# Kernel tuning notes

Hardware: AMD Instinct MI355X
Metric: run time of the kernel (lower is better)

Reference implementation:

```python
import jax, jax.numpy as jnp
import numpy as np

N_NODES, N_EDGES, HIDDEN, N_GRAPHS, TARGET, DEPTH, N_FOURIER = 20000, 320000, 128, 64, 32, 4, 4


def setup_inputs() -> dict:
    key = jax.random.key(0)
    ks = iter(jax.random.split(key, 48))
    H, L = HIDDEN, DEPTH

    def nrm(shape, fan):
        return jax.random.normal(next(ks), shape, jnp.float32) / np.sqrt(fan)

    inp = {}
    inp["x"] = jnp.zeros((N_NODES, 9), jnp.int32)  # only N is used (use_node_features=False)
    src = jax.random.randint(next(ks), (N_EDGES,), 0, N_NODES, dtype=jnp.int32)
    dst = jax.random.randint(next(ks), (N_EDGES,), 0, N_NODES, dtype=jnp.int32)
    inp["edge_index"] = jnp.stack([src, dst])  # row0 = x_j (source), row1 = x_i (target)
    inp["edge_attr"] = jax.random.uniform(next(ks), (N_EDGES,), jnp.float32) * 5.0  # distances
    inp["batch"] = ((jnp.arange(N_NODES) * N_GRAPHS) // N_NODES).astype(jnp.int32)  # sorted, all graphs non-empty

    ein = 2 * N_FOURIER + 1
    inp["node_embedding"] = jax.random.normal(next(ks), (H,), jnp.float32)
    inp["edge_W"] = nrm((ein, H), ein); inp["edge_b"] = jnp.zeros((H,), jnp.float32)
    # stacked per-mp-layer params (scanned over)
    inp["msg_W1"] = nrm((L, 3 * H, H), 3 * H); inp["msg_b1"] = jnp.zeros((L, H), jnp.float32)
    inp["msg_W2"] = nrm((L, H, H), H);        inp["msg_b2"] = jnp.zeros((L, H), jnp.float32)
    inp["soft_W"] = nrm((L, H, 1), H);        inp["soft_b"] = jnp.zeros((L, 1), jnp.float32)
    inp["upd_W1"] = nrm((L, H, H), H);        inp["upd_b1"] = jnp.zeros((L, H), jnp.float32)
    inp["upd_W2"] = nrm((L, H, H), H);        inp["upd_b2"] = jnp.zeros((L, H), jnp.float32)
    # node-wise output MLP (2 layers, last_activation=None)
    inp["no_W1"] = nrm((H, H), H); inp["no_b1"] = jnp.zeros((H,), jnp.float32)
    inp["no_W2"] = nrm((H, H), H); inp["no_b2"] = jnp.zeros((H,), jnp.float32)
    # readout MLP: in = 3*H (mean, sum, max), hidden = H, out = TARGET
    inp["out_W1"] = nrm((3 * H, H), 3 * H); inp["out_b1"] = jnp.zeros((H,), jnp.float32)
    inp["out_W2"] = nrm((H, TARGET), H);    inp["out_b2"] = jnp.zeros((TARGET,), jnp.float32)
    return inp


def _forward(x, edge_index, edge_attr, batch, node_embedding, edge_W, edge_b,
             msg_W1, msg_b1, msg_W2, msg_b2, soft_W, soft_b,
             upd_W1, upd_b1, upd_W2, upd_b2,
             no_W1, no_b1, no_W2, no_b2, out_W1, out_b1, out_W2, out_b2):
    N = x.shape[0]
    silu = jax.nn.silu
    h = jnp.broadcast_to(node_embedding, (N, node_embedding.shape[0]))

    # fourier_encode_dist: [E] -> [E, 2*F+1]
    scales = 2.0 ** jnp.arange(N_FOURIER, dtype=edge_attr.dtype)
    d = edge_attr[:, None] / scales
    e = jnp.concatenate([jnp.sin(d), jnp.cos(d), edge_attr[:, None]], axis=-1)
    # edge_input MLP (layers=1, last_activation=SiLU) followed by extra F.silu in forward
    e = silu(silu(e @ edge_W + edge_b))

    src, dst = edge_index[0], edge_index[1]  # x_j gathers src, x_i gathers dst

    def layer(carry, p):
        h, e = carry
        W1, b1, W2, b2, sW, sb, uW1, ub1, uW2, ub2 = p
        m_in = jnp.concatenate([h[src], h[dst], e], axis=-1)  # [x_j, x_i, edge_attr]
        m = silu(silu(m_in @ W1 + b1) @ W2 + b2)              # message MLP, last_activation=SiLU
        e = e + m                                             # in-place edge_attr += message
        w = jax.nn.sigmoid(m @ sW + sb)                       # soft edge gate
        agg = jax.ops.segment_sum(m * w, dst, num_segments=N) # aggr='sum' to targets
        hn = silu((agg + h) @ uW1 + ub1) @ uW2 + ub2          # update MLP, last_activation=None
        return (h + hn, e), None

    (h, e), _ = jax.lax.scan(layer, (h, e),
                             (msg_W1, msg_b1, msg_W2, msg_b2, soft_W, soft_b,
                              upd_W1, upd_b1, upd_W2, upd_b2))

    h = silu(h @ no_W1 + no_b1) @ no_W2 + no_b2  # node-wise output network

    G = N_GRAPHS
    s = jax.ops.segment_sum(h, batch, num_segments=G)
    cnt = jax.ops.segment_sum(jnp.ones((N, 1), h.dtype), batch, num_segments=G)
    mean = s / jnp.maximum(cnt, 1.0)
    mx = jax.ops.segment_max(h, batch, num_segments=G)
    readout = jnp.concatenate([mean, s, mx], axis=-1)  # aggregators = [mean, sum, max]
    return jax.nn.relu(readout @ out_W1 + out_b1) @ out_W2 + out_b2


def reference(x, edge_index, edge_attr, batch, node_embedding, edge_W, edge_b,
              msg_W1, msg_b1, msg_W2, msg_b2, soft_W, soft_b,
              upd_W1, upd_b1, upd_W2, upd_b2,
              no_W1, no_b1, no_W2, no_b2, out_W1, out_b1, out_W2, out_b2):
    return _forward(x, edge_index, edge_attr, batch, node_embedding, edge_W, edge_b,
                    msg_W1, msg_b1, msg_W2, msg_b2, soft_W, soft_b,
                    upd_W1, upd_b1, upd_W2, upd_b2,
                    no_W1, no_b1, no_W2, no_b2, out_W1, out_b1, out_W2, out_b2)
```

## Files before the change

### kernel.cpp

```cpp
#include <hip/hip_runtime.h>

#define N_NODES 20000
#define N_EDGES 320000
#define HID 128
#define NG 64
#define TGT 32
#define DEPTHL 4

typedef __attribute__((ext_vector_type(8))) short s16x8;
typedef __attribute__((ext_vector_type(4))) short s16x4;
typedef __attribute__((ext_vector_type(4))) float f32x4;

__device__ __forceinline__ unsigned short f2b(float f) {
  unsigned u = __builtin_bit_cast(unsigned, f);
  u = (u + 0x7FFFu + ((u >> 16) & 1u)) >> 16;
  return (unsigned short)u;
}
__device__ __forceinline__ float b2f(unsigned short s) {
  return __builtin_bit_cast(float, ((unsigned)s) << 16);
}
__device__ __forceinline__ float silu_f(float x) { return x / (1.f + __expf(-x)); }

__device__ __forceinline__ unsigned fkey(float f) {
  unsigned u = __builtin_bit_cast(unsigned, f);
  return (u & 0x80000000u) ? ~u : (u | 0x80000000u);
}
__device__ __forceinline__ float unkey(unsigned k) {
  unsigned u = (k & 0x80000000u) ? (k ^ 0x80000000u) : ~k;
  return __builtin_bit_cast(float, u);
}

__device__ __forceinline__ f32x4 mfma16(s16x8 a, s16x8 b, f32x4 c) {
  return __builtin_amdgcn_mfma_f32_16x16x32_bf16(a, b, c, 0, 0, 0);
}

__device__ __forceinline__ void lds_fence() {
  asm volatile("s_waitcnt lgkmcnt(0)" ::: "memory");
  __builtin_amdgcn_sched_barrier(0);
}

__device__ __forceinline__ s16x8 pack8(float4 a, float4 b) {
  s16x8 p;
  p[0]=(short)f2b(a.x); p[1]=(short)f2b(a.y); p[2]=(short)f2b(a.z); p[3]=(short)f2b(a.w);
  p[4]=(short)f2b(b.x); p[5]=(short)f2b(b.y); p[6]=(short)f2b(b.z); p[7]=(short)f2b(b.w);
  return p;
}

__global__ void pack_weights(const float* __restrict__ mW1, const float* __restrict__ mW2,
                             const float* __restrict__ uW1, const float* __restrict__ uW2,
                             const float* __restrict__ nW1, const float* __restrict__ nW2,
                             short* __restrict__ pW1, short* __restrict__ pW2,
                             short* __restrict__ puW1, short* __restrict__ puW2,
                             short* __restrict__ pnW1, short* __restrict__ pnW2) {
  int i = blockIdx.x * 256 + threadIdx.x;
  const float* src; short* dst; int K, r;
  if (i < 196608)      { src = mW1 + (i/49152)*49152; dst = pW1 + i;            r = i % 49152; K = 384; }
  else if (i < 262144) { int q = i - 196608; src = mW2 + (q/16384)*16384; dst = pW2  + q; r = q % 16384; K = 128; }
  else if (i < 327680) { int q = i - 262144; src = uW1 + (q/16384)*16384; dst = puW1 + q; r = q % 16384; K = 128; }
  else if (i < 393216) { int q = i - 327680; src = uW2 + (q/16384)*16384; dst = puW2 + q; r = q % 16384; K = 128; }
  else if (i < 409600) { int q = i - 393216; src = nW1; dst = pnW1 + q; r = q; K = 128; }
  else if (i < 425984) { int q = i - 409600; src = nW2; dst = pnW2 + q; r = q; K = 128; }
  else return;
  int j = r & 7, lane = (r >> 3) & 63, q2 = r >> 9;
  int KT = K >> 5;
  int kt = q2 % KT, ct = q2 / KT;
  int k = kt*32 + ((lane >> 4) << 3) + j;
  int col = ct*16 + (lane & 15);
  dst[0] = (short)f2b(src[k*HID + col]);
}

__global__ void sort_init(int* __restrict__ hist, int* __restrict__ cursor) {
  int i = blockIdx.x * 256 + threadIdx.x;
  if (i < N_NODES) { hist[i] = 0; cursor[i] = 0; }
}

__global__ void hist_kernel(const int* __restrict__ dst, int* __restrict__ hist) {
  int e = blockIdx.x * 256 + threadIdx.x;
  if (e < N_EDGES) atomicAdd(&hist[dst[e]], 1);
}

__global__ __launch_bounds__(1024) void scan_kernel(const int* __restrict__ hist,
                                                    int* __restrict__ offs) {
  __shared__ int part[1024];
  int t = threadIdx.x;
  int base = t * 20;
  int loc[20];
  int s = 0;
#pragma unroll
  for (int i = 0; i < 20; ++i) {
    loc[i] = s;
    int n = base + i;
    s += (n < N_NODES ? hist[n] : 0);
  }
  part[t] = s;
  __syncthreads();
  for (int st = 1; st < 1024; st <<= 1) {
    int v = (t >= st) ? part[t - st] : 0;
    __syncthreads();
    part[t] += v;
    __syncthreads();
  }
  int pre = (t > 0) ? part[t - 1] : 0;
#pragma unroll
  for (int i = 0; i < 20; ++i) {
    int n = base + i;
    if (n < N_NODES) offs[n] = pre + loc[i];
  }
}

__global__ void scatter_kernel(const int* __restrict__ src, const int* __restrict__ dst,
                               const float* __restrict__ ea, const int* __restrict__ offs,
                               int* __restrict__ cursor,
                               unsigned short* __restrict__ ssrc,
                               unsigned short* __restrict__ sdst,
                               float* __restrict__ sea) {
  int e = blockIdx.x * 256 + threadIdx.x;
  if (e >= N_EDGES) return;
  int d = dst[e];
  int pos = offs[d] + atomicAdd(&cursor[d], 1);
  ssrc[pos] = (unsigned short)src[e];
  sdst[pos] = (unsigned short)d;
  sea[pos] = ea[e];
}

__global__ void edge_init(const float* __restrict__ sea, const float* __restrict__ eW,
                          const float* __restrict__ eb, unsigned short* __restrict__ e) {
  __shared__ float feat[2][9];
  int t = threadIdx.x;
  int le = t >> 7, c = t & 127;
  int edge = blockIdx.x * 2 + le;
  if (c < 9) {
    float d = sea[edge];
    float sc = (float)(1 << (c & 3));
    float v;
    if (c < 4) v = sinf(d / sc);
    else if (c < 8) v = cosf(d / sc);
    else v = d;
    feat[le][c] = v;
  }
  __syncthreads();
  float acc = eb[c];
#pragma unroll
  for (int j = 0; j < 9; ++j) acc += feat[le][j] * eW[j*HID + c];
  acc = silu_f(silu_f(acc));
  e[edge*HID + c] = f2b(acc);
}

__global__ void init_h(float* __restrict__ h, const float* __restrict__ ne,
                       float* __restrict__ agg, unsigned short* __restrict__ hb) {
  int i = blockIdx.x * 256 + threadIdx.x;
  if (i < N_NODES * HID) {
    float v = ne[i & 127];
    h[i] = v; hb[i] = f2b(v); agg[i] = 0.f;
  }
}

__global__ void init_read(float* __restrict__ s, float* __restrict__ cnt, unsigned* __restrict__ mx) {
  int i = blockIdx.x * 256 + threadIdx.x;
  if (i < NG * HID) { s[i] = 0.f; mx[i] = 0x007FFFFFu; }
  if (i < NG) cnt[i] = 0.f;
}

__global__ __launch_bounds__(256) void msg_kernel(
    const unsigned short* __restrict__ hb, unsigned short* __restrict__ e,
    const unsigned short* __restrict__ ssrc, const unsigned short* __restrict__ sdst,
    const short* __restrict__ W1p, const float* __restrict__ b1,
    const short* __restrict__ W2p, const float* __restrict__ b2,
    const float* __restrict__ sW, const float* __restrict__ sbp,
    float* __restrict__ agg) {
  __shared__ __align__(16) short t1f[4][2048];
  int t = threadIdx.x;
  int wv = t >> 6, lane = t & 63;
  int l15 = lane & 15, hi = lane >> 4;
  int edge = blockIdx.x * 64 + wv * 16 + l15;
  int si = ssrc[edge];
  int d  = sdst[edge];

  s16x8 bfrag[12];
#pragma unroll
  for (int kt = 0; kt < 4; ++kt)
    bfrag[kt] = *(const s16x8*)(hb + si*HID + kt*32 + hi*8);
#pragma unroll
  for (int kt = 0; kt < 4; ++kt)
    bfrag[4+kt] = *(const s16x8*)(hb + d*HID + kt*32 + hi*8);
#pragma unroll
  for (int kt = 0; kt < 4; ++kt)
    bfrag[8+kt] = *(const s16x8*)(e + (size_t)edge*HID + kt*32 + hi*8);

  f32x4 acc1[8];
#pragma unroll
  for (int ct = 0; ct < 8; ++ct) acc1[ct] = f32x4{0.f, 0.f, 0.f, 0.f};
#pragma unroll
  for (int kt = 0; kt < 12; ++kt) {
#pragma unroll
    for (int ct = 0; ct < 8; ++ct) {
      s16x8 afr = *(const s16x8*)(W1p + ((ct*12 + kt)*64 + lane)*8);
      acc1[ct] = mfma16(afr, bfrag[kt], acc1[ct]);
    }
  }
  short* myt1 = &t1f[wv][0];
#pragma unroll
  for (int ct = 0; ct < 8; ++ct) {
    f32x4 bias = *(const f32x4*)(b1 + ct*16 + hi*4);
    s16x4 pk4;
#pragma unroll
    for (int r = 0; r < 4; ++r) pk4[r] = (short)f2b(silu_f(acc1[ct][r] + bias[r]));
    *(s16x4*)&myt1[((2*ct + (hi >> 1))*16 + l15)*8 + (hi & 1)*4] = pk4;
  }
  uint2 eold[8];
#pragma unroll
  for (int ct = 0; ct < 8; ++ct)
    eold[ct] = *(const uint2*)(e + (size_t)edge*HID + ct*16 + hi*4);
  lds_fence();

  f32x4 acc2[8];
#pragma unroll
  for (int ct = 0; ct < 8; ++ct) acc2[ct] = f32x4{0.f, 0.f, 0.f, 0.f};
#pragma unroll
  for (int kt = 0; kt < 4; ++kt) {
    s16x8 bfr = *(const s16x8*)&myt1[((kt*4 + hi)*16 + l15)*8];
#pragma unroll
    for (int ct = 0; ct < 8; ++ct) {
      s16x8 afr = *(const s16x8*)(W2p + ((ct*4 + kt)*64 + lane)*8);
      acc2[ct] = mfma16(afr, bfr, acc2[ct]);
    }
  }
  float m[8][4];
  float wpart = 0.f;
#pragma unroll
  for (int ct = 0; ct < 8; ++ct) {
    f32x4 bias = *(const f32x4*)(b2 + ct*16 + hi*4);
    f32x4 swv  = *(const f32x4*)(sW + ct*16 + hi*4);
#pragma unroll
    for (int r = 0; r < 4; ++r) {
      float mv = silu_f(acc2[ct][r] + bias[r]);
      m[ct][r] = mv;
      wpart += mv * swv[r];
    }
  }
  wpart += __shfl_xor(wpart, 16);
  wpart += __shfl_xor(wpart, 32);
  float wg = 1.f / (1.f + __expf(-(wpart + sbp[0])));

  int pd = __shfl_up(d, 1, 16);
  bool head = (l15 == 0) || (pd != d);
  int okbits = 0;
#pragma unroll
  for (int i = 0; i < 4; ++i) {
    int off = 1 << i;
    int nd = __shfl_down(d, off, 16);
    if ((l15 + off < 16) && (nd == d)) okbits |= (1 << i);
  }
  float* aggrow = agg + d*HID;

#pragma unroll
  for (int ct = 0; ct < 8; ++ct) {
    uint2 cur = eold[ct];
    float f0 = b2f((unsigned short)(cur.x & 0xFFFFu)) + m[ct][0];
    float f1 = b2f((unsigned short)(cur.x >> 16))     + m[ct][1];
    float f2v = b2f((unsigned short)(cur.y & 0xFFFFu)) + m[ct][2];
    float f3 = b2f((unsigned short)(cur.y >> 16))     + m[ct][3];
    uint2 nw;
    nw.x = (unsigned)f2b(f0)  | ((unsigned)f2b(f1) << 16);
    nw.y = (unsigned)f2b(f2v) | ((unsigned)f2b(f3) << 16);
    *(uint2*)(e + (size_t)edge*HID + ct*16 + hi*4) = nw;

    f32x4 v;
#pragma unroll
    for (int r = 0; r < 4; ++r) v[r] = m[ct][r] * wg;
#pragma unroll
    for (int i = 0; i < 4; ++i) {
      int off = 1 << i;
      bool ok = (okbits >> i) & 1;
#pragma unroll
      for (int r = 0; r < 4; ++r) {
        float nv = __shfl_down(v[r], off, 16);
        if (ok) v[r] += nv;
      }
    }
    if (head) {
      float* ap = aggrow + ct*16 + hi*4;
      atomicAdd(ap + 0, v[0]);
      atomicAdd(ap + 1, v[1]);
      atomicAdd(ap + 2, v[2]);
      atomicAdd(ap + 3, v[3]);
    }
  }
}

template<int MODE>
__global__ __launch_bounds__(256) void node_kernel(
    float* __restrict__ h, float* __restrict__ agg,
    const short* __restrict__ W1p, const float* __restrict__ b1,
    const short* __restrict__ W2p, const float* __restrict__ b2,
    float* __restrict__ out, unsigned short* __restrict__ hb) {
  __shared__ __align__(16) short t1f[4][2048];
  int t = threadIdx.x;
  int wv = t >> 6, lane = t & 63;
  int l15 = lane & 15, hi = lane >> 4;
  int node = blockIdx.x * 64 + wv * 16 + l15;
  bool valid = node < N_NODES;
  int nodec = valid ? node : (N_NODES - 1);

  s16x8 bfrag[4];
#pragma unroll
  for (int kt = 0; kt < 4; ++kt) {
    const float* hp = h + nodec*HID + kt*32 + hi*8;
    float4 v0 = *(const float4*)hp;
    float4 v1 = *(const float4*)(hp + 4);
    if (MODE == 0) {
      float* ap = agg + nodec*HID + kt*32 + hi*8;
      float4 a0 = *(const float4*)ap;
      float4 a1 = *(const float4*)(ap + 4);
      v0.x += a0.x; v0.y += a0.y; v0.z += a0.z; v0.w += a0.w;
      v1.x += a1.x; v1.y += a1.y; v1.z += a1.z; v1.w += a1.w;
      if (valid) {
        float4 z = {0.f, 0.f, 0.f, 0.f};
        *(float4*)ap = z;
        *(float4*)(ap + 4) = z;
      }
    }
    bfrag[kt] = pack8(v0, v1);
  }

  f32x4 acc1[8];
#pragma unroll
  for (int ct = 0; ct < 8; ++ct) acc1[ct] = f32x4{0.f, 0.f, 0.f, 0.f};
#pragma unroll
  for (int kt = 0; kt < 4; ++kt) {
#pragma unroll
    for (int ct = 0; ct < 8; ++ct) {
      s16x8 afr = *(const s16x8*)(W1p + ((ct*4 + kt)*64 + lane)*8);
      acc1[ct] = mfma16(afr, bfrag[kt], acc1[ct]);
    }
  }
  short* myt1 = &t1f[wv][0];
#pragma unroll
  for (int ct = 0; ct < 8; ++ct) {
    f32x4 bias = *(const f32x4*)(b1 + ct*16 + hi*4);
    s16x4 pk4;
#pragma unroll
    for (int r = 0; r < 4; ++r) pk4[r] = (short)f2b(silu_f(acc1[ct][r] + bias[r]));
    *(s16x4*)&myt1[((2*ct + (hi >> 1))*16 + l15)*8 + (hi & 1)*4] = pk4;
  }
  lds_fence();

  f32x4 acc2[8];
#pragma unroll
  for (int ct = 0; ct < 8; ++ct) acc2[ct] = f32x4{0.f, 0.f, 0.f, 0.f};
#pragma unroll
  for (int kt = 0; kt < 4; ++kt) {
    s16x8 bfr = *(const s16x8*)&myt1[((kt*4 + hi)*16 + l15)*8];
#pragma unroll
    for (int ct = 0; ct < 8; ++ct) {
      s16x8 afr = *(const s16x8*)(W2p + ((ct*4 + kt)*64 + lane)*8);
      acc2[ct] = mfma16(afr, bfr, acc2[ct]);
    }
  }
  if (valid) {
#pragma unroll
    for (int ct = 0; ct < 8; ++ct) {
      f32x4 bias = *(const f32x4*)(b2 + ct*16 + hi*4);
      float* op = (MODE == 0 ? h : out) + node*HID + ct*16 + hi*4;
      float4 res;
      if (MODE == 0) {
        float4 cur = *(const float4*)op;
        res.x = cur.x + acc2[ct][0] + bias[0];
        res.y = cur.y + acc2[ct][1] + bias[1];
        res.z = cur.z + acc2[ct][2] + bias[2];
        res.w = cur.w + acc2[ct][3] + bias[3];
      } else {
        res.x = acc2[ct][0] + bias[0];
        res.y = acc2[ct][1] + bias[1];
        res.z = acc2[ct][2] + bias[2];
        res.w = acc2[ct][3] + bias[3];
      }
      *(float4*)op = res;
      if (MODE == 0) {
        uint2 nb;
        nb.x = (unsigned)f2b(res.x) | ((unsigned)f2b(res.y) << 16);
        nb.y = (unsigned)f2b(res.z) | ((unsigned)f2b(res.w) << 16);
        *(uint2*)(hb + node*HID + ct*16 + hi*4) = nb;
      }
    }
  }
}

__global__ void accum_kernel(const float* __restrict__ h2, const int* __restrict__ batch,
                             float* __restrict__ s, float* __restrict__ cnt,
                             unsigned* __restrict__ mx) {
  int c = threadIdx.x & 127;
  int lr = threadIdx.x >> 7;
  int base = blockIdx.x * 64;
  int cur = -1; float sum = 0.f, mxv = -3.0e38f, count = 0.f;
  for (int i = 0; i < 32; ++i) {
    int node = base + lr + 2 * i;
    if (node >= N_NODES) break;
    int g = batch[node];
    if (g != cur) {
      if (cur >= 0) {
        atomicAdd(&s[cur*HID + c], sum);
        atomicMax(&mx[cur*HID + c], fkey(mxv));
        if (c == 0) atomicAdd(&cnt[cur], count);
      }
      cur = g; sum = 0.f; mxv = -3.0e38f; count = 0.f;
    }
    float v = h2[node*HID + c];
    sum += v; mxv = fmaxf(mxv, v); count += 1.f;
  }
  if (cur >= 0) {
    atomicAdd(&s[cur*HID + c], sum);
    atomicMax(&mx[cur*HID + c], fkey(mxv));
    if (c == 0) atomicAdd(&cnt[cur], count);
  }
}

__global__ void final_kernel(const float* __restrict__ s, const float* __restrict__ cnt,
                             const unsigned* __restrict__ mx,
                             const float* __restrict__ W1, const float* __restrict__ b1,
                             const float* __restrict__ W2, const float* __restrict__ b2,
                             float* __restrict__ out) {
  __shared__ float ro[3 * HID];
  __shared__ float r1[HID];
  int g = blockIdx.x, c = threadIdx.x;
  float sv = s[g*HID + c];
  float cn = cnt[g];
  ro[c] = sv / fmaxf(cn, 1.f);
  ro[HID + c] = sv;
  ro[2*HID + c] = unkey(mx[g*HID + c]);
  __syncthreads();
  float acc = b1[c];
  for (int k = 0; k < 3*HID; ++k) acc += ro[k] * W1[k*HID + c];
  r1[c] = fmaxf(acc, 0.f);
  __syncthreads();
  if (c < TGT) {
    float o = b2[c];
    for (int k = 0; k < HID; ++k) o += r1[k] * W2[k*TGT + c];
    out[g*TGT + c] = o;
  }
}

extern "C" void kernel_launch(void* const* d_in, const int* in_sizes, int n_in,
                              void* d_out, int out_size, void* d_ws, size_t ws_size,
                              hipStream_t stream) {
  const int*   eidx = (const int*)d_in[1];
  const int*   srci = eidx;
  const int*   dsti = eidx + N_EDGES;
  const float* ea   = (const float*)d_in[2];
  const int*   batch= (const int*)d_in[3];
  const float* nemb = (const float*)d_in[4];
  const float* eW   = (const float*)d_in[5];
  const float* eb   = (const float*)d_in[6];
  const float* mW1  = (const float*)d_in[7];
  const float* mb1  = (const float*)d_in[8];
  const float* mW2  = (const float*)d_in[9];
  const float* mb2  = (const float*)d_in[10];
  const float* sW   = (const float*)d_in[11];
  const float* sb   = (const float*)d_in[12];
  const float* uW1  = (const float*)d_in[13];
  const float* ub1  = (const float*)d_in[14];
  const float* uW2  = (const float*)d_in[15];
  const float* ub2  = (const float*)d_in[16];
  const float* nW1  = (const float*)d_in[17];
  const float* nb1  = (const float*)d_in[18];
  const float* nW2  = (const float*)d_in[19];
  const float* nb2  = (const float*)d_in[20];
  const float* oW1  = (const float*)d_in[21];
  const float* ob1  = (const float*)d_in[22];
  const float* oW2  = (const float*)d_in[23];
  const float* ob2  = (const float*)d_in[24];

  char* ws = (char*)d_ws;
  float* sbuf = (float*)(ws + 0);
  float* cnt  = (float*)(ws + 32768);
  unsigned* mx= (unsigned*)(ws + 33024);
  short* pW1  = (short*)(ws + 65792);
  short* pW2  = (short*)(ws + 459008);
  short* puW1 = (short*)(ws + 590080);
  short* puW2 = (short*)(ws + 721152);
  short* pnW1 = (short*)(ws + 852224);
  short* pnW2 = (short*)(ws + 884992);
  int* hist   = (int*)(ws + 917760);
  int* cursor = (int*)(ws + 997760);
  int* offs   = (int*)(ws + 1077760);
  unsigned short* ssrc = (unsigned short*)(ws + 1157760);
  unsigned short* sdst = (unsigned short*)(ws + 1797760);
  float* sea  = (float*)(ws + 2437760);
  unsigned short* e = (unsigned short*)(ws + 3717760);
  float* h    = (float*)(ws + 85637760);
  float* agg  = (float*)(ws + 95877760);
  unsigned short* hb = (unsigned short*)(ws + 106117760);
  float* h2   = agg;

  sort_init<<<(N_NODES + 255) / 256, 256, 0, stream>>>(hist, cursor);
  hist_kernel<<<N_EDGES / 256, 256, 0, stream>>>(dsti, hist);
  scan_kernel<<<1, 1024, 0, stream>>>(hist, offs);
  scatter_kernel<<<N_EDGES / 256, 256, 0, stream>>>(srci, dsti, ea, offs, cursor,
                                                    ssrc, sdst, sea);

  pack_weights<<<1664, 256, 0, stream>>>(mW1, mW2, uW1, uW2, nW1, nW2,
                                         pW1, pW2, puW1, puW2, pnW1, pnW2);
  edge_init<<<N_EDGES / 2, 256, 0, stream>>>(sea, eW, eb, e);
  init_h<<<(N_NODES * HID) / 256, 256, 0, stream>>>(h, nemb, agg, hb);
  init_read<<<33, 256, 0, stream>>>(sbuf, cnt, mx);

  for (int l = 0; l < DEPTHL; ++l) {
    msg_kernel<<<N_EDGES / 64, 256, 0, stream>>>(hb, e, ssrc, sdst,
        pW1 + l*49152, mb1 + l*HID, pW2 + l*16384, mb2 + l*HID,
        sW + l*HID, sb + l, agg);
    node_kernel<0><<<(N_NODES + 63) / 64, 256, 0, stream>>>(h, agg,
        puW1 + l*16384, ub1 + l*HID, puW2 + l*16384, ub2 + l*HID, nullptr, hb);
  }
  node_kernel<1><<<(N_NODES + 63) / 64, 256, 0, stream>>>(h, nullptr,
      pnW1, nb1, pnW2, nb2, h2, nullptr);
  accum_kernel<<<(N_NODES + 63) / 64, 256, 0, stream>>>(h2, batch, sbuf, cnt, mx);
  final_kernel<<<NG, 128, 0, stream>>>(sbuf, cnt, mx, oW1, ob1, oW2, ob2, (float*)d_out);
}
```

Measured before the change: 979.4 us.

## Make message kernel persistent with LDS-resident weights and double-buffered edge loads

The message kernel now launches 256 blocks of 512 threads. Each block first copies the packed bf16 W1/W2 of the layer (144 KB, now stored contiguously per layer) into shared memory. Each wave then processes 10 consecutive 16-edge tiles, prefetching the gathered node and edge fragments of the next tile while the current one computes. This replaces the per-MFMA global/L2 weight fragment reads and spreads the weight load over many tiles. The cost is a large LDS footprint that allows only one block per CU, very low wave occupancy, high register pressure from the two fragment buffers, and a second-layer MFMA split into halves to fit a smaller per-wave staging buffer.

```diff
diff --git a/kernel.cpp b/kernel.cpp
--- a/kernel.cpp
+++ b/kernel.cpp
@@ -6,6 +6,7 @@
 #define NG 64
 #define TGT 32
 #define DEPTHL 4
+#define NTILES 20000
 
 typedef __attribute__((ext_vector_type(8))) short s16x8;
 typedef __attribute__((ext_vector_type(4))) short s16x4;
@@ -49,13 +50,13 @@
 __global__ void pack_weights(const float* __restrict__ mW1, const float* __restrict__ mW2,
                              const float* __restrict__ uW1, const float* __restrict__ uW2,
                              const float* __restrict__ nW1, const float* __restrict__ nW2,
-                             short* __restrict__ pW1, short* __restrict__ pW2,
+                             short* __restrict__ pMsg,
                              short* __restrict__ puW1, short* __restrict__ puW2,
                              short* __restrict__ pnW1, short* __restrict__ pnW2) {
   int i = blockIdx.x * 256 + threadIdx.x;
   const float* src; short* dst; int K, r;
-  if (i < 196608)      { src = mW1 + (i/49152)*49152; dst = pW1 + i;            r = i % 49152; K = 384; }
-  else if (i < 262144) { int q = i - 196608; src = mW2 + (q/16384)*16384; dst = pW2  + q; r = q % 16384; K = 128; }
+  if (i < 196608)      { int l = i/49152; r = i % 49152; src = mW1 + l*49152; dst = pMsg + l*65536 + r;        K = 384; }
+  else if (i < 262144) { int q = i - 196608; int l = q/16384; r = q % 16384; src = mW2 + l*16384; dst = pMsg + l*65536 + 49152 + r; K = 128; }
   else if (i < 327680) { int q = i - 262144; src = uW1 + (q/16384)*16384; dst = puW1 + q; r = q % 16384; K = 128; }
   else if (i < 393216) { int q = i - 327680; src = uW2 + (q/16384)*16384; dst = puW2 + q; r = q % 16384; K = 128; }
   else if (i < 409600) { int q = i - 393216; src = nW1; dst = pnW1 + q; r = q; K = 128; }
@@ -161,130 +162,172 @@
   if (i < NG) cnt[i] = 0.f;
 }
 
-__global__ __launch_bounds__(256) void msg_kernel(
+__global__ __launch_bounds__(512, 2) void msg_kernel(
     const unsigned short* __restrict__ hb, unsigned short* __restrict__ e,
     const unsigned short* __restrict__ ssrc, const unsigned short* __restrict__ sdst,
-    const short* __restrict__ W1p, const float* __restrict__ b1,
-    const short* __restrict__ W2p, const float* __restrict__ b2,
+    const short* __restrict__ Wp, const float* __restrict__ b1,
+    const float* __restrict__ b2,
     const float* __restrict__ sW, const float* __restrict__ sbp,
     float* __restrict__ agg) {
-  __shared__ __align__(16) short t1f[4][2048];
+  __shared__ __align__(16) short smem[73728];
+  short* sW1 = smem;
+  short* sW2 = smem + 49152;
   int t = threadIdx.x;
   int wv = t >> 6, lane = t & 63;
   int l15 = lane & 15, hi = lane >> 4;
-  int edge = blockIdx.x * 64 + wv * 16 + l15;
-  int si = ssrc[edge];
-  int d  = sdst[edge];
-
-  s16x8 bfrag[12];
-#pragma unroll
-  for (int kt = 0; kt < 4; ++kt)
-    bfrag[kt] = *(const s16x8*)(hb + si*HID + kt*32 + hi*8);
-#pragma unroll
-  for (int kt = 0; kt < 4; ++kt)
-    bfrag[4+kt] = *(const s16x8*)(hb + d*HID + kt*32 + hi*8);
-#pragma unroll
-  for (int kt = 0; kt < 4; ++kt)
-    bfrag[8+kt] = *(const s16x8*)(e + (size_t)edge*HID + kt*32 + hi*8);
-
-  f32x4 acc1[8];
-#pragma unroll
-  for (int ct = 0; ct < 8; ++ct) acc1[ct] = f32x4{0.f, 0.f, 0.f, 0.f};
-#pragma unroll
-  for (int kt = 0; kt < 12; ++kt) {
+  short* myt1 = smem + 65536 + wv * 1024;
+
+  {
+    const s16x8* Wg = (const s16x8*)Wp;
+    s16x8* Wl = (s16x8*)smem;
+    for (int i = t; i < 8192; i += 512) Wl[i] = Wg[i];
+  }
+  __syncthreads();
+
+  float sb_v = sbp[0];
+  int wgid = blockIdx.x * 8 + wv;
+  int tile0 = wgid * 10;
+
+  s16x8 bfA[12], bfB[12];
+  int dA = 0, dB = 0;
+
+  auto loadb = [&](s16x8* B, int& D, int tile) {
+    int edge = tile * 16 + l15;
+    int si = ssrc[edge]; D = sdst[edge];
+#pragma unroll
+    for (int kt = 0; kt < 4; ++kt)
+      B[kt] = *(const s16x8*)(hb + si*HID + kt*32 + hi*8);
+#pragma unroll
+    for (int kt = 0; kt < 4; ++kt)
+      B[4+kt] = *(const s16x8*)(hb + D*HID + kt*32 + hi*8);
+#pragma unroll
+    for (int kt = 0; kt < 4; ++kt)
+      B[8+kt] = *(const s16x8*)(e + (size_t)edge*HID + kt*32 + hi*8);
+  };
+
+  auto body = [&](int tile, const s16x8* bfrag, int d) {
+    int edge = tile * 16 + l15;
+    uint2 eold[8];
+#pragma unroll
+    for (int ct = 0; ct < 8; ++ct)
+      eold[ct] = *(const uint2*)(e + (size_t)edge*HID + ct*16 + hi*4);
+
+    f32x4 acc1[8];
+#pragma unroll
+    for (int ct = 0; ct < 8; ++ct) acc1[ct] = f32x4{0.f, 0.f, 0.f, 0.f};
+#pragma unroll
+    for (int kt = 0; kt < 12; ++kt) {
+#pragma unroll
+      for (int ct = 0; ct < 8; ++ct) {
+        s16x8 afr = *(const s16x8*)&sW1[((ct*12 + kt)*64 + lane)*8];
+        acc1[ct] = mfma16(afr, bfrag[kt], acc1[ct]);
+      }
+    }
+
+    f32x4 acc2[8];
+#pragma unroll
+    for (int ct = 0; ct < 8; ++ct) acc2[ct] = f32x4{0.f, 0.f, 0.f, 0.f};
+#pragma unroll
+    for (int p = 0; p < 2; ++p) {
+#pragma unroll
+      for (int c4 = 0; c4 < 4; ++c4) {
+        int ct = 4*p + c4;
+        f32x4 bias = *(const f32x4*)(b1 + ct*16 + hi*4);
+        s16x4 pk4;
+#pragma unroll
+        for (int r = 0; r < 4; ++r) pk4[r] = (short)f2b(silu_f(acc1[ct][r] + bias[r]));
+        *(s16x4*)&myt1[((2*c4 + (hi >> 1))*16 + l15)*8 + (hi & 1)*4] = pk4;
+      }
+      lds_fence();
+#pragma unroll
+      for (int k2 = 0; k2 < 2; ++k2) {
+        int kt = 2*p + k2;
+        s16x8 bfr = *(const s16x8*)&myt1[((k2*4 + hi)*16 + l15)*8];
+#pragma unroll
+        for (int ct = 0; ct < 8; ++ct) {
+          s16x8 afr = *(const s16x8*)&sW2[((ct*4 + kt)*64 + lane)*8];
+          acc2[ct] = mfma16(afr, bfr, acc2[ct]);
+        }
+      }
+      lds_fence();
+    }
+
+    float m[8][4];
+    float wpart = 0.f;
 #pragma unroll
     for (int ct = 0; ct < 8; ++ct) {
-      s16x8 afr = *(const s16x8*)(W1p + ((ct*12 + kt)*64 + lane)*8);
-      acc1[ct] = mfma16(afr, bfrag[kt], acc1[ct]);
-    }
-  }
-  short* myt1 = &t1f[wv][0];
-#pragma unroll
-  for (int ct = 0; ct < 8; ++ct) {
-    f32x4 bias = *(const f32x4*)(b1 + ct*16 + hi*4);
-    s16x4 pk4;
-#pragma unroll
-    for (int r = 0; r < 4; ++r) pk4[r] = (short)f2b(silu_f(acc1[ct][r] + bias[r]));
-    *(s16x4*)&myt1[((2*ct + (hi >> 1))*16 + l15)*8 + (hi & 1)*4] = pk4;
-  }
-  uint2 eold[8];
-#pragma unroll
-  for (int ct = 0; ct < 8; ++ct)
-    eold[ct] = *(const uint2*)(e + (size_t)edge*HID + ct*16 + hi*4);
-  lds_fence();
-
-  f32x4 acc2[8];
-#pragma unroll
-  for (int ct = 0; ct < 8; ++ct) acc2[ct] = f32x4{0.f, 0.f, 0.f, 0.f};
-#pragma unroll
-  for (int kt = 0; kt < 4; ++kt) {
-    s16x8 bfr = *(const s16x8*)&myt1[((kt*4 + hi)*16 + l15)*8];
-#pragma unroll
-    for (int ct = 0; ct < 8; ++ct) {
-      s16x8 afr = *(const s16x8*)(W2p + ((ct*4 + kt)*64 + lane)*8);
-      acc2[ct] = mfma16(afr, bfr, acc2[ct]);
-    }
-  }
-  float m[8][4];
-  float wpart = 0.f;
-#pragma unroll
-  for (int ct = 0; ct < 8; ++ct) {
-    f32x4 bias = *(const f32x4*)(b2 + ct*16 + hi*4);
-    f32x4 swv  = *(const f32x4*)(sW + ct*16 + hi*4);
-#pragma unroll
-    for (int r = 0; r < 4; ++r) {
-      float mv = silu_f(acc2[ct][r] + bias[r]);
-      m[ct][r] = mv;
-      wpart += mv * swv[r];
-    }
-  }
-  wpart += __shfl_xor(wpart, 16);
-  wpart += __shfl_xor(wpart, 32);
-  float wg = 1.f / (1.f + __expf(-(wpart + sbp[0])));
-
-  int pd = __shfl_up(d, 1, 16);
-  bool head = (l15 == 0) || (pd != d);
-  int okbits = 0;
-#pragma unroll
-  for (int i = 0; i < 4; ++i) {
-    int off = 1 << i;
-    int nd = __shfl_down(d, off, 16);
-    if ((l15 + off < 16) && (nd == d)) okbits |= (1 << i);
-  }
-  float* aggrow = agg + d*HID;
-
-#pragma unroll
-  for (int ct = 0; ct < 8; ++ct) {
-    uint2 cur = eold[ct];
-    float f0 = b2f((unsigned short)(cur.x & 0xFFFFu)) + m[ct][0];
-    float f1 = b2f((unsigned short)(cur.x >> 16))     + m[ct][1];
-    float f2v = b2f((unsigned short)(cur.y & 0xFFFFu)) + m[ct][2];
-    float f3 = b2f((unsigned short)(cur.y >> 16))     + m[ct][3];
-    uint2 nw;
-    nw.x = (unsigned)f2b(f0)  | ((unsigned)f2b(f1) << 16);
-    nw.y = (unsigned)f2b(f2v) | ((unsigned)f2b(f3) << 16);
-    *(uint2*)(e + (size_t)edge*HID + ct*16 + hi*4) = nw;
-
-    f32x4 v;
-#pragma unroll
-    for (int r = 0; r < 4; ++r) v[r] = m[ct][r] * wg;
+      f32x4 bias = *(const f32x4*)(b2 + ct*16 + hi*4);
+      f32x4 swv  = *(const f32x4*)(sW + ct*16 + hi*4);
+#pragma unroll
+      for (int r = 0; r < 4; ++r) {
+        float mv = silu_f(acc2[ct][r] + bias[r]);
+        m[ct][r] = mv;
+        wpart += mv * swv[r];
+      }
+    }
+    wpart += __shfl_xor(wpart, 16);
+    wpart += __shfl_xor(wpart, 32);
+    float wg = 1.f / (1.f + __expf(-(wpart + sb_v)));
+
+    int pd = __shfl_up(d, 1, 16);
+    bool head = (l15 == 0) || (pd != d);
+    int okbits = 0;
 #pragma unroll
     for (int i = 0; i < 4; ++i) {
       int off = 1 << i;
-      bool ok = (okbits >> i) & 1;
-#pragma unroll
-      for (int r = 0; r < 4; ++r) {
-        float nv = __shfl_down(v[r], off, 16);
-        if (ok) v[r] += nv;
-      }
-    }
-    if (head) {
-      float* ap = aggrow + ct*16 + hi*4;
-      atomicAdd(ap + 0, v[0]);
-      atomicAdd(ap + 1, v[1]);
-      atomicAdd(ap + 2, v[2]);
-      atomicAdd(ap + 3, v[3]);
-    }
+      int nd = __shfl_down(d, off, 16);
+      if ((l15 + off < 16) && (nd == d)) okbits |= (1 << i);
+    }
+    float* aggrow = agg + d*HID;
+
+#pragma unroll
+    for (int ct = 0; ct < 8; ++ct) {
+      uint2 cur = eold[ct];
+      float f0 = b2f((unsigned short)(cur.x & 0xFFFFu)) + m[ct][0];
+      float f1 = b2f((unsigned short)(cur.x >> 16))     + m[ct][1];
+      float f2v = b2f((unsigned short)(cur.y & 0xFFFFu)) + m[ct][2];
+      float f3 = b2f((unsigned short)(cur.y >> 16))     + m[ct][3];
+      uint2 nw;
+      nw.x = (unsigned)f2b(f0)  | ((unsigned)f2b(f1) << 16);
+      nw.y = (unsigned)f2b(f2v) | ((unsigned)f2b(f3) << 16);
+      *(uint2*)(e + (size_t)edge*HID + ct*16 + hi*4) = nw;
+
+      f32x4 v;
+#pragma unroll
+      for (int r = 0; r < 4; ++r) v[r] = m[ct][r] * wg;
+#pragma unroll
+      for (int i = 0; i < 4; ++i) {
+        int off = 1 << i;
+        bool ok = (okbits >> i) & 1;
+#pragma unroll
+        for (int r = 0; r < 4; ++r) {
+          float nv = __shfl_down(v[r], off, 16);
+          if (ok) v[r] += nv;
+        }
+      }
+      if (head) {
+        float* ap = aggrow + ct*16 + hi*4;
+        atomicAdd(ap + 0, v[0]);
+        atomicAdd(ap + 1, v[1]);
+        atomicAdd(ap + 2, v[2]);
+        atomicAdd(ap + 3, v[3]);
+      }
+    }
+  };
+
+  if (tile0 >= NTILES) return;
+  loadb(bfA, dA, tile0);
+#pragma unroll 1
+  for (int i = 0; i < 10; i += 2) {
+    int ta = tile0 + i;
+    if (ta >= NTILES) break;
+    int tb = ta + 1;
+    if (tb < NTILES && tb < tile0 + 10) loadb(bfB, dB, tb);
+    body(ta, bfA, dA);
+    if (tb >= NTILES || tb >= tile0 + 10) break;
+    int tc = tb + 1;
+    if (tc < NTILES && tc < tile0 + 10) loadb(bfA, dA, tc);
+    body(tb, bfB, dB);
   }
 }
 
@@ -474,8 +517,7 @@
   float* sbuf = (float*)(ws + 0);
   float* cnt  = (float*)(ws + 32768);
   unsigned* mx= (unsigned*)(ws + 33024);
-  short* pW1  = (short*)(ws + 65792);
-  short* pW2  = (short*)(ws + 459008);
+  short* pMsg = (short*)(ws + 65792);
   short* puW1 = (short*)(ws + 590080);
   short* puW2 = (short*)(ws + 721152);
   short* pnW1 = (short*)(ws + 852224);
@@ -499,14 +541,14 @@
                                                     ssrc, sdst, sea);
 
   pack_weights<<<1664, 256, 0, stream>>>(mW1, mW2, uW1, uW2, nW1, nW2,
-                                         pW1, pW2, puW1, puW2, pnW1, pnW2);
+                                         pMsg, puW1, puW2, pnW1, pnW2);
   edge_init<<<N_EDGES / 2, 256, 0, stream>>>(sea, eW, eb, e);
   init_h<<<(N_NODES * HID) / 256, 256, 0, stream>>>(h, nemb, agg, hb);
   init_read<<<33, 256, 0, stream>>>(sbuf, cnt, mx);
 
   for (int l = 0; l < DEPTHL; ++l) {
-    msg_kernel<<<N_EDGES / 64, 256, 0, stream>>>(hb, e, ssrc, sdst,
-        pW1 + l*49152, mb1 + l*HID, pW2 + l*16384, mb2 + l*HID,
+    msg_kernel<<<256, 512, 0, stream>>>(hb, e, ssrc, sdst,
+        pMsg + l*65536, mb1 + l*HID, mb2 + l*HID,
         sW + l*HID, sb + l, agg);
     node_kernel<0><<<(N_NODES + 63) / 64, 256, 0, stream>>>(h, agg,
         puW1 + l*16384, ub1 + l*HID, puW2 + l*16384, ub2 + l*HID, nullptr, hb);
```

Measured after the change: 930.4 us. -5.0%, faster.

## Replace atomic scatter aggregation with per-edge message buffer and CSR gather

Applied to the files above, without the earlier changes.

The message kernel no longer reduces within a segment and issues float atomics into a node aggregate buffer. It instead writes each gated message as bf16 to a per-edge buffer in destination-sorted order. The node kernel then gathers each node's incoming messages using the CSR offsets and degrees. This removes the atomics and the zeroing of the aggregate buffer, at the cost of an extra 80MB bf16 write and read per layer, bf16 rounding of messages before summation, and divergent per-node degree loops. The msg W1 and W2 packed weights are also merged into one contiguous per-layer block.

```diff
diff --git a/kernel.cpp b/kernel.cpp
--- a/kernel.cpp
+++ b/kernel.cpp
@@ -49,13 +49,13 @@
 __global__ void pack_weights(const float* __restrict__ mW1, const float* __restrict__ mW2,
                              const float* __restrict__ uW1, const float* __restrict__ uW2,
                              const float* __restrict__ nW1, const float* __restrict__ nW2,
-                             short* __restrict__ pW1, short* __restrict__ pW2,
+                             short* __restrict__ pMsg,
                              short* __restrict__ puW1, short* __restrict__ puW2,
                              short* __restrict__ pnW1, short* __restrict__ pnW2) {
   int i = blockIdx.x * 256 + threadIdx.x;
   const float* src; short* dst; int K, r;
-  if (i < 196608)      { src = mW1 + (i/49152)*49152; dst = pW1 + i;            r = i % 49152; K = 384; }
-  else if (i < 262144) { int q = i - 196608; src = mW2 + (q/16384)*16384; dst = pW2  + q; r = q % 16384; K = 128; }
+  if (i < 196608)      { int l = i/49152; r = i % 49152; src = mW1 + l*49152; dst = pMsg + l*65536 + r;        K = 384; }
+  else if (i < 262144) { int q = i - 196608; int l = q/16384; r = q % 16384; src = mW2 + l*16384; dst = pMsg + l*65536 + 49152 + r; K = 128; }
   else if (i < 327680) { int q = i - 262144; src = uW1 + (q/16384)*16384; dst = puW1 + q; r = q % 16384; K = 128; }
   else if (i < 393216) { int q = i - 327680; src = uW2 + (q/16384)*16384; dst = puW2 + q; r = q % 16384; K = 128; }
   else if (i < 409600) { int q = i - 393216; src = nW1; dst = pnW1 + q; r = q; K = 128; }
@@ -147,11 +147,11 @@
 }
 
 __global__ void init_h(float* __restrict__ h, const float* __restrict__ ne,
-                       float* __restrict__ agg, unsigned short* __restrict__ hb) {
+                       unsigned short* __restrict__ hb) {
   int i = blockIdx.x * 256 + threadIdx.x;
   if (i < N_NODES * HID) {
     float v = ne[i & 127];
-    h[i] = v; hb[i] = f2b(v); agg[i] = 0.f;
+    h[i] = v; hb[i] = f2b(v);
   }
 }
 
@@ -164,11 +164,13 @@
 __global__ __launch_bounds__(256) void msg_kernel(
     const unsigned short* __restrict__ hb, unsigned short* __restrict__ e,
     const unsigned short* __restrict__ ssrc, const unsigned short* __restrict__ sdst,
-    const short* __restrict__ W1p, const float* __restrict__ b1,
-    const short* __restrict__ W2p, const float* __restrict__ b2,
+    const short* __restrict__ Wp, const float* __restrict__ b1,
+    const float* __restrict__ b2,
     const float* __restrict__ sW, const float* __restrict__ sbp,
-    float* __restrict__ agg) {
+    unsigned short* __restrict__ mw) {
   __shared__ __align__(16) short t1f[4][2048];
+  const short* W1p = Wp;
+  const short* W2p = Wp + 49152;
   int t = threadIdx.x;
   int wv = t >> 6, lane = t & 63;
   int l15 = lane & 15, hi = lane >> 4;
@@ -241,17 +243,6 @@
   wpart += __shfl_xor(wpart, 16);
   wpart += __shfl_xor(wpart, 32);
   float wg = 1.f / (1.f + __expf(-(wpart + sbp[0])));
-
-  int pd = __shfl_up(d, 1, 16);
-  bool head = (l15 == 0) || (pd != d);
-  int okbits = 0;
-#pragma unroll
-  for (int i = 0; i < 4; ++i) {
-    int off = 1 << i;
-    int nd = __shfl_down(d, off, 16);
-    if ((l15 + off < 16) && (nd == d)) okbits |= (1 << i);
-  }
-  float* aggrow = agg + d*HID;
 
 #pragma unroll
   for (int ct = 0; ct < 8; ++ct) {
@@ -265,32 +256,17 @@
     nw.y = (unsigned)f2b(f2v) | ((unsigned)f2b(f3) << 16);
     *(uint2*)(e + (size_t)edge*HID + ct*16 + hi*4) = nw;
 
-    f32x4 v;
-#pragma unroll
-    for (int r = 0; r < 4; ++r) v[r] = m[ct][r] * wg;
-#pragma unroll
-    for (int i = 0; i < 4; ++i) {
-      int off = 1 << i;
-      bool ok = (okbits >> i) & 1;
-#pragma unroll
-      for (int r = 0; r < 4; ++r) {
-        float nv = __shfl_down(v[r], off, 16);
-        if (ok) v[r] += nv;
-      }
-    }
-    if (head) {
-      float* ap = aggrow + ct*16 + hi*4;
-      atomicAdd(ap + 0, v[0]);
-      atomicAdd(ap + 1, v[1]);
-      atomicAdd(ap + 2, v[2]);
-      atomicAdd(ap + 3, v[3]);
-    }
+    uint2 wout;
+    wout.x = (unsigned)f2b(m[ct][0]*wg) | ((unsigned)f2b(m[ct][1]*wg) << 16);
+    wout.y = (unsigned)f2b(m[ct][2]*wg) | ((unsigned)f2b(m[ct][3]*wg) << 16);
+    *(uint2*)(mw + (size_t)edge*HID + ct*16 + hi*4) = wout;
   }
 }
 
 template<int MODE>
 __global__ __launch_bounds__(256) void node_kernel(
-    float* __restrict__ h, float* __restrict__ agg,
+    float* __restrict__ h, const unsigned short* __restrict__ mw,
+    const int* __restrict__ offs, const int* __restrict__ hist,
     const short* __restrict__ W1p, const float* __restrict__ b1,
     const short* __restrict__ W2p, const float* __restrict__ b2,
     float* __restrict__ out, unsigned short* __restrict__ hb) {
@@ -303,24 +279,45 @@
   int nodec = valid ? node : (N_NODES - 1);
 
   s16x8 bfrag[4];
-#pragma unroll
-  for (int kt = 0; kt < 4; ++kt) {
-    const float* hp = h + nodec*HID + kt*32 + hi*8;
-    float4 v0 = *(const float4*)hp;
-    float4 v1 = *(const float4*)(hp + 4);
-    if (MODE == 0) {
-      float* ap = agg + nodec*HID + kt*32 + hi*8;
-      float4 a0 = *(const float4*)ap;
-      float4 a1 = *(const float4*)(ap + 4);
-      v0.x += a0.x; v0.y += a0.y; v0.z += a0.z; v0.w += a0.w;
-      v1.x += a1.x; v1.y += a1.y; v1.z += a1.z; v1.w += a1.w;
-      if (valid) {
-        float4 z = {0.f, 0.f, 0.f, 0.f};
-        *(float4*)ap = z;
-        *(float4*)(ap + 4) = z;
+  if (MODE == 0) {
+    int beg = offs[nodec];
+    int deg = valid ? hist[nodec] : 0;
+    int dmax = deg;
+#pragma unroll
+    for (int o = 32; o; o >>= 1) dmax = max(dmax, __shfl_xor(dmax, o));
+    float sum[4][8];
+#pragma unroll
+    for (int kt = 0; kt < 4; ++kt)
+#pragma unroll
+      for (int j = 0; j < 8; ++j) sum[kt][j] = 0.f;
+    for (int j = 0; j < dmax; ++j) {
+      if (j < deg) {
+        size_t row = (size_t)(beg + j) * HID;
+#pragma unroll
+        for (int kt = 0; kt < 4; ++kt) {
+          s16x8 v = *(const s16x8*)(mw + row + kt*32 + hi*8);
+#pragma unroll
+          for (int q = 0; q < 8; ++q) sum[kt][q] += b2f((unsigned short)v[q]);
+        }
       }
     }
-    bfrag[kt] = pack8(v0, v1);
+#pragma unroll
+    for (int kt = 0; kt < 4; ++kt) {
+      const float* hp = h + nodec*HID + kt*32 + hi*8;
+      float4 v0 = *(const float4*)hp;
+      float4 v1 = *(const float4*)(hp + 4);
+      v0.x += sum[kt][0]; v0.y += sum[kt][1]; v0.z += sum[kt][2]; v0.w += sum[kt][3];
+      v1.x += sum[kt][4]; v1.y += sum[kt][5]; v1.z += sum[kt][6]; v1.w += sum[kt][7];
+      bfrag[kt] = pack8(v0, v1);
+    }
+  } else {
+#pragma unroll
+    for (int kt = 0; kt < 4; ++kt) {
+      const float* hp = h + nodec*HID + kt*32 + hi*8;
+      float4 v0 = *(const float4*)hp;
+      float4 v1 = *(const float4*)(hp + 4);
+      bfrag[kt] = pack8(v0, v1);
+    }
   }
 
   f32x4 acc1[8];
@@ -474,8 +471,7 @@
   float* sbuf = (float*)(ws + 0);
   float* cnt  = (float*)(ws + 32768);
   unsigned* mx= (unsigned*)(ws + 33024);
-  short* pW1  = (short*)(ws + 65792);
-  short* pW2  = (short*)(ws + 459008);
+  short* pMsg = (short*)(ws + 65792);
   short* puW1 = (short*)(ws + 590080);
   short* puW2 = (short*)(ws + 721152);
   short* pnW1 = (short*)(ws + 852224);
@@ -488,9 +484,9 @@
   float* sea  = (float*)(ws + 2437760);
   unsigned short* e = (unsigned short*)(ws + 3717760);
   float* h    = (float*)(ws + 85637760);
-  float* agg  = (float*)(ws + 95877760);
-  unsigned short* hb = (unsigned short*)(ws + 106117760);
-  float* h2   = agg;
+  unsigned short* hb = (unsigned short*)(ws + 95877760);
+  unsigned short* mw = (unsigned short*)(ws + 100997760);
+  float* h2   = (float*)mw;
 
   sort_init<<<(N_NODES + 255) / 256, 256, 0, stream>>>(hist, cursor);
   hist_kernel<<<N_EDGES / 256, 256, 0, stream>>>(dsti, hist);
@@ -499,19 +495,19 @@
                                                     ssrc, sdst, sea);
 
   pack_weights<<<1664, 256, 0, stream>>>(mW1, mW2, uW1, uW2, nW1, nW2,
-                                         pW1, pW2, puW1, puW2, pnW1, pnW2);
+                                         pMsg, puW1, puW2, pnW1, pnW2);
   edge_init<<<N_EDGES / 2, 256, 0, stream>>>(sea, eW, eb, e);
-  init_h<<<(N_NODES * HID) / 256, 256, 0, stream>>>(h, nemb, agg, hb);
+  init_h<<<(N_NODES * HID) / 256, 256, 0, stream>>>(h, nemb, hb);
   init_read<<<33, 256, 0, stream>>>(sbuf, cnt, mx);
 
   for (int l = 0; l < DEPTHL; ++l) {
     msg_kernel<<<N_EDGES / 64, 256, 0, stream>>>(hb, e, ssrc, sdst,
-        pW1 + l*49152, mb1 + l*HID, pW2 + l*16384, mb2 + l*HID,
-        sW + l*HID, sb + l, agg);
-    node_kernel<0><<<(N_NODES + 63) / 64, 256, 0, stream>>>(h, agg,
+        pMsg + l*65536, mb1 + l*HID, mb2 + l*HID,
+        sW + l*HID, sb + l, mw);
+    node_kernel<0><<<(N_NODES + 63) / 64, 256, 0, stream>>>(h, mw, offs, hist,
         puW1 + l*16384, ub1 + l*HID, puW2 + l*16384, ub2 + l*HID, nullptr, hb);
   }
-  node_kernel<1><<<(N_NODES + 63) / 64, 256, 0, stream>>>(h, nullptr,
+  node_kernel<1><<<(N_NODES + 63) / 64, 256, 0, stream>>>(h, nullptr, nullptr, nullptr,
       pnW1, nb1, pnW2, nb2, h2, nullptr);
   accum_kernel<<<(N_NODES + 63) / 64, 256, 0, stream>>>(h2, batch, sbuf, cnt, mx);
   final_kernel<<<NG, 128, 0, stream>>>(sbuf, cnt, mx, oW1, ob1, oW2, ob2, (float*)d_out);
```

Measured after the change: 1.009 ms. 3.0% more time.

## Cut msg_kernel register pressure to raise occupancy and merge per-layer message weights

Applied to the files above, without the earlier changes.

The message kernel now loads the three 128-wide input chunks (source, destination, edge) in turn instead of holding all twelve fragments at once. It also defers the old-edge reload until after the second GEMM and recomputes the silu messages rather than keeping a 32-float array, and asks for 8 waves per EU via launch bounds. The per-layer W1 and W2 packed weights are placed in one contiguous buffer. This aims to raise occupancy and hide gather latency, at the cost of recomputed silu, less load-level parallelism per wave, and possible spills under the tighter register cap.

```diff
diff --git a/kernel.cpp b/kernel.cpp
--- a/kernel.cpp
+++ b/kernel.cpp
@@ -49,13 +49,13 @@
 __global__ void pack_weights(const float* __restrict__ mW1, const float* __restrict__ mW2,
                              const float* __restrict__ uW1, const float* __restrict__ uW2,
                              const float* __restrict__ nW1, const float* __restrict__ nW2,
-                             short* __restrict__ pW1, short* __restrict__ pW2,
+                             short* __restrict__ pMsg,
                              short* __restrict__ puW1, short* __restrict__ puW2,
                              short* __restrict__ pnW1, short* __restrict__ pnW2) {
   int i = blockIdx.x * 256 + threadIdx.x;
   const float* src; short* dst; int K, r;
-  if (i < 196608)      { src = mW1 + (i/49152)*49152; dst = pW1 + i;            r = i % 49152; K = 384; }
-  else if (i < 262144) { int q = i - 196608; src = mW2 + (q/16384)*16384; dst = pW2  + q; r = q % 16384; K = 128; }
+  if (i < 196608)      { int l = i/49152; r = i % 49152; src = mW1 + l*49152; dst = pMsg + l*65536 + r;        K = 384; }
+  else if (i < 262144) { int q = i - 196608; int l = q/16384; r = q % 16384; src = mW2 + l*16384; dst = pMsg + l*65536 + 49152 + r; K = 128; }
   else if (i < 327680) { int q = i - 262144; src = uW1 + (q/16384)*16384; dst = puW1 + q; r = q % 16384; K = 128; }
   else if (i < 393216) { int q = i - 327680; src = uW2 + (q/16384)*16384; dst = puW2 + q; r = q % 16384; K = 128; }
   else if (i < 409600) { int q = i - 393216; src = nW1; dst = pnW1 + q; r = q; K = 128; }
@@ -161,14 +161,16 @@
   if (i < NG) cnt[i] = 0.f;
 }
 
-__global__ __launch_bounds__(256) void msg_kernel(
+__global__ __launch_bounds__(256, 8) void msg_kernel(
     const unsigned short* __restrict__ hb, unsigned short* __restrict__ e,
     const unsigned short* __restrict__ ssrc, const unsigned short* __restrict__ sdst,
-    const short* __restrict__ W1p, const float* __restrict__ b1,
-    const short* __restrict__ W2p, const float* __restrict__ b2,
+    const short* __restrict__ Wp, const float* __restrict__ b1,
+    const float* __restrict__ b2,
     const float* __restrict__ sW, const float* __restrict__ sbp,
     float* __restrict__ agg) {
   __shared__ __align__(16) short t1f[4][2048];
+  const short* W1p = Wp;
+  const short* W2p = Wp + 49152;
   int t = threadIdx.x;
   int wv = t >> 6, lane = t & 63;
   int l15 = lane & 15, hi = lane >> 4;
@@ -176,28 +178,44 @@
   int si = ssrc[edge];
   int d  = sdst[edge];
 
-  s16x8 bfrag[12];
-#pragma unroll
-  for (int kt = 0; kt < 4; ++kt)
-    bfrag[kt] = *(const s16x8*)(hb + si*HID + kt*32 + hi*8);
-#pragma unroll
-  for (int kt = 0; kt < 4; ++kt)
-    bfrag[4+kt] = *(const s16x8*)(hb + d*HID + kt*32 + hi*8);
-#pragma unroll
-  for (int kt = 0; kt < 4; ++kt)
-    bfrag[8+kt] = *(const s16x8*)(e + (size_t)edge*HID + kt*32 + hi*8);
-
   f32x4 acc1[8];
 #pragma unroll
   for (int ct = 0; ct < 8; ++ct) acc1[ct] = f32x4{0.f, 0.f, 0.f, 0.f};
-#pragma unroll
-  for (int kt = 0; kt < 12; ++kt) {
-#pragma unroll
-    for (int ct = 0; ct < 8; ++ct) {
-      s16x8 afr = *(const s16x8*)(W1p + ((ct*12 + kt)*64 + lane)*8);
-      acc1[ct] = mfma16(afr, bfrag[kt], acc1[ct]);
-    }
-  }
+
+  {
+    s16x8 bf[4];
+#pragma unroll
+    for (int kt = 0; kt < 4; ++kt)
+      bf[kt] = *(const s16x8*)(hb + si*HID + kt*32 + hi*8);
+#pragma unroll
+    for (int kt = 0; kt < 4; ++kt)
+#pragma unroll
+      for (int ct = 0; ct < 8; ++ct)
+        acc1[ct] = mfma16(*(const s16x8*)(W1p + ((ct*12 + kt)*64 + lane)*8), bf[kt], acc1[ct]);
+  }
+  {
+    s16x8 bf[4];
+#pragma unroll
+    for (int kt = 0; kt < 4; ++kt)
+      bf[kt] = *(const s16x8*)(hb + d*HID + kt*32 + hi*8);
+#pragma unroll
+    for (int kt = 0; kt < 4; ++kt)
+#pragma unroll
+      for (int ct = 0; ct < 8; ++ct)
+        acc1[ct] = mfma16(*(const s16x8*)(W1p + ((ct*12 + kt + 4)*64 + lane)*8), bf[kt], acc1[ct]);
+  }
+  {
+    s16x8 bf[4];
+#pragma unroll
+    for (int kt = 0; kt < 4; ++kt)
+      bf[kt] = *(const s16x8*)(e + (size_t)edge*HID + kt*32 + hi*8);
+#pragma unroll
+    for (int kt = 0; kt < 4; ++kt)
+#pragma unroll
+      for (int ct = 0; ct < 8; ++ct)
+        acc1[ct] = mfma16(*(const s16x8*)(W1p + ((ct*12 + kt + 8)*64 + lane)*8), bf[kt], acc1[ct]);
+  }
+
   short* myt1 = &t1f[wv][0];
 #pragma unroll
   for (int ct = 0; ct < 8; ++ct) {
@@ -207,10 +225,6 @@
     for (int r = 0; r < 4; ++r) pk4[r] = (short)f2b(silu_f(acc1[ct][r] + bias[r]));
     *(s16x4*)&myt1[((2*ct + (hi >> 1))*16 + l15)*8 + (hi & 1)*4] = pk4;
   }
-  uint2 eold[8];
-#pragma unroll
-  for (int ct = 0; ct < 8; ++ct)
-    eold[ct] = *(const uint2*)(e + (size_t)edge*HID + ct*16 + hi*4);
   lds_fence();
 
   f32x4 acc2[8];
@@ -225,18 +239,20 @@
       acc2[ct] = mfma16(afr, bfr, acc2[ct]);
     }
   }
-  float m[8][4];
+
+  uint2 eold[8];
+#pragma unroll
+  for (int ct = 0; ct < 8; ++ct)
+    eold[ct] = *(const uint2*)(e + (size_t)edge*HID + ct*16 + hi*4);
+
   float wpart = 0.f;
 #pragma unroll
   for (int ct = 0; ct < 8; ++ct) {
     f32x4 bias = *(const f32x4*)(b2 + ct*16 + hi*4);
     f32x4 swv  = *(const f32x4*)(sW + ct*16 + hi*4);
 #pragma unroll
-    for (int r = 0; r < 4; ++r) {
-      float mv = silu_f(acc2[ct][r] + bias[r]);
-      m[ct][r] = mv;
-      wpart += mv * swv[r];
-    }
+    for (int r = 0; r < 4; ++r)
+      wpart += silu_f(acc2[ct][r] + bias[r]) * swv[r];
   }
   wpart += __shfl_xor(wpart, 16);
   wpart += __shfl_xor(wpart, 32);
@@ -255,11 +271,16 @@
 
 #pragma unroll
   for (int ct = 0; ct < 8; ++ct) {
+    f32x4 bias = *(const f32x4*)(b2 + ct*16 + hi*4);
+    f32x4 mv;
+#pragma unroll
+    for (int r = 0; r < 4; ++r) mv[r] = silu_f(acc2[ct][r] + bias[r]);
+
     uint2 cur = eold[ct];
-    float f0 = b2f((unsigned short)(cur.x & 0xFFFFu)) + m[ct][0];
-    float f1 = b2f((unsigned short)(cur.x >> 16))     + m[ct][1];
-    float f2v = b2f((unsigned short)(cur.y & 0xFFFFu)) + m[ct][2];
-    float f3 = b2f((unsigned short)(cur.y >> 16))     + m[ct][3];
+    float f0 = b2f((unsigned short)(cur.x & 0xFFFFu)) + mv[0];
+    float f1 = b2f((unsigned short)(cur.x >> 16))     + mv[1];
+    float f2v = b2f((unsigned short)(cur.y & 0xFFFFu)) + mv[2];
+    float f3 = b2f((unsigned short)(cur.y >> 16))     + mv[3];
     uint2 nw;
     nw.x = (unsigned)f2b(f0)  | ((unsigned)f2b(f1) << 16);
     nw.y = (unsigned)f2b(f2v) | ((unsigned)f2b(f3) << 16);
@@ -267,7 +288,7 @@
 
     f32x4 v;
 #pragma unroll
-    for (int r = 0; r < 4; ++r) v[r] = m[ct][r] * wg;
+    for (int r = 0; r < 4; ++r) v[r] = mv[r] * wg;
 #pragma unroll
     for (int i = 0; i < 4; ++i) {
       int off = 1 << i;
@@ -474,8 +495,7 @@
   float* sbuf = (float*)(ws + 0);
   float* cnt  = (float*)(ws + 32768);
   unsigned* mx= (unsigned*)(ws + 33024);
-  short* pW1  = (short*)(ws + 65792);
-  short* pW2  = (short*)(ws + 459008);
+  short* pMsg = (short*)(ws + 65792);
   short* puW1 = (short*)(ws + 590080);
   short* puW2 = (short*)(ws + 721152);
   short* pnW1 = (short*)(ws + 852224);
@@ -499,14 +519,14 @@
                                                     ssrc, sdst, sea);
 
   pack_weights<<<1664, 256, 0, stream>>>(mW1, mW2, uW1, uW2, nW1, nW2,
-                                         pW1, pW2, puW1, puW2, pnW1, pnW2);
+                                         pMsg, puW1, puW2, pnW1, pnW2);
   edge_init<<<N_EDGES / 2, 256, 0, stream>>>(sea, eW, eb, e);
   init_h<<<(N_NODES * HID) / 256, 256, 0, stream>>>(h, nemb, agg, hb);
   init_read<<<33, 256, 0, stream>>>(sbuf, cnt, mx);
 
   for (int l = 0; l < DEPTHL; ++l) {
     msg_kernel<<<N_EDGES / 64, 256, 0, stream>>>(hb, e, ssrc, sdst,
-        pW1 + l*49152, mb1 + l*HID, pW2 + l*16384, mb2 + l*HID,
+        pMsg + l*65536, mb1 + l*HID, mb2 + l*HID,
         sW + l*HID, sb + l, agg);
     node_kernel<0><<<(N_NODES + 63) / 64, 256, 0, stream>>>(h, agg,
         puW1 + l*16384, ub1 + l*HID, puW2 + l*16384, ub2 + l*HID, nullptr, hb);
```

Measured after the change: 1.172 ms. 1.2x slower.
